# Performance work log

Measured on AMD Instinct MI355X. Metric: run time of the kernel, lower is better.

## Reference

```python
import jax, jax.numpy as jnp
import numpy as np

N_NODES = 100000
N_EDGES = 6400000
F_IN = 128
F_OUT = 16


def setup_inputs() -> dict:
    key = jax.random.key(0)
    k1, k2, k3 = jax.random.split(key, 3)
    x = jax.random.normal(k1, (N_NODES, F_IN), dtype=jnp.float32)
    edge_index = jax.random.randint(k2, (2, N_EDGES), 0, N_NODES, dtype=jnp.int64)
    W = jax.random.normal(k3, (F_IN, F_OUT), dtype=jnp.float32) / np.sqrt(F_IN)
    b = jnp.zeros((F_OUT,), dtype=jnp.float32)
    return {"x": x, "edge_index": edge_index, "W": W, "b": b}


def reference(x, edge_index, W, b):
    # GCNConv (PyG defaults: add self-loops, symmetric normalization) -> tanh -> mean pool
    N = x.shape[0]
    loops = jnp.arange(N, dtype=edge_index.dtype)
    row = jnp.concatenate([edge_index[0], loops])  # source nodes
    col = jnp.concatenate([edge_index[1], loops])  # target nodes
    # degree of target nodes (edge weight 1.0)
    deg = jax.ops.segment_sum(jnp.ones(row.shape[0], dtype=x.dtype), col, num_segments=N)
    dinv = jnp.where(deg > 0, jax.lax.rsqrt(deg), 0.0)
    norm = dinv[row] * dinv[col]  # [E+N]
    h = x @ W  # [N, F_OUT] transform first (cheaper than transforming messages)
    msgs = h[row] * norm[:, None]  # gather + scale
    out = jax.ops.segment_sum(msgs, col, num_segments=N) + b  # scatter-add
    h = jnp.tanh(out)
    # MeanAggregation over all nodes -> single graph embedding [1, F_OUT]
    return jnp.mean(h, axis=0, keepdims=True)
```

## Files before the change

kernel.cpp:

```cpp
#include <hip/hip_runtime.h>
#include <math.h>

#define N_NODES 100000
#define N_EDGES 6400000
#define F_IN 128
#define F_OUT 16
#define NB 391
#define NBLK 1600
#define EPB 4000
#define LOCW 392
#define KPB 4
#define ACCN (NB * 256 * F_OUT)
#define QSCALE 1024.0f
#define QINV   (1.0f / 1024.0f)
#define FIN_GRID 640

__global__ void __launch_bounds__(256) count_kernel(const int* __restrict__ col,
                                                    int* __restrict__ loc,
                                                    int* __restrict__ deg) {
    __shared__ int hist[NB];
    const int t = threadIdx.x, k = blockIdx.x;
    const int z0 = k * 63;
    for (int j = t; j < 63; j += 256)
        if (z0 + j < N_NODES) deg[z0 + j] = 0;
    for (int i = t; i < NB; i += 256) hist[i] = 0;
    __syncthreads();
    const int e0 = k * EPB;
    for (int i = t; i < EPB; i += 256) atomicAdd(&hist[col[e0 + i] >> 8], 1);
    __syncthreads();
    for (int b = t; b < NB; b += 256) loc[k * LOCW + b] = hist[b];
}

__global__ void __launch_bounds__(256) desta_kernel(const int* __restrict__ loc,
        int* __restrict__ destT, int* __restrict__ total) {
    __shared__ int tsum[256];
    const int t = threadIdx.x, b = blockIdx.x;
    int v[7]; int s = 0;
    #pragma unroll
    for (int j = 0; j < 7; j++) {
        int k = t * 7 + j;
        v[j] = (k < NBLK) ? loc[k * LOCW + b] : 0;
        s += v[j];
    }
    tsum[t] = s;
    __syncthreads();
    for (int off = 1; off < 256; off <<= 1) {
        int a = (t >= off) ? tsum[t - off] : 0;
        __syncthreads();
        tsum[t] += a;
        __syncthreads();
    }
    int run = tsum[t] - s;
    #pragma unroll
    for (int j = 0; j < 7; j++) {
        int k = t * 7 + j;
        if (k < NBLK) destT[(size_t)b * NBLK + k] = run;
        run += v[j];
    }
    if (t == 255) total[b] = tsum[255];
}

__global__ void destb_kernel(const int* __restrict__ total, int* __restrict__ boffs) {
    __shared__ int lds[512];
    const int t = threadIdx.x;
    int v = (t < NB) ? total[t] : 0;
    lds[t] = v; __syncthreads();
    for (int off = 1; off < 512; off <<= 1) {
        int a = (t >= off) ? lds[t - off] : 0; __syncthreads();
        lds[t] += a; __syncthreads();
    }
    if (t < NB) boffs[t] = lds[t] - v;
    if (t == NB) boffs[NB] = N_EDGES;
}

__global__ void __launch_bounds__(256) place_kernel(const int* __restrict__ row,
        const int* __restrict__ col, const int* __restrict__ destT,
        const int* __restrict__ boffs, unsigned int* __restrict__ packed) {
    __shared__ int hist[NB];
    __shared__ int scanb[512];
    __shared__ int base[NB];
    __shared__ int gadj[NB];
    __shared__ unsigned int tile[EPB];
    __shared__ unsigned short tileb[EPB];
    const int t = threadIdx.x, k = blockIdx.x;
    const int e0 = k * EPB;
    int myc[16], myr[16];
    #pragma unroll
    for (int j = 0; j < 16; j++) {
        int idx = t + j * 256;
        if (idx < EPB) { myc[j] = col[e0 + idx]; myr[j] = row[e0 + idx]; }
        else { myc[j] = -1; myr[j] = 0; }
    }
    for (int i = t; i < NB; i += 256) hist[i] = 0;
    __syncthreads();
    #pragma unroll
    for (int j = 0; j < 16; j++)
        if (myc[j] >= 0) atomicAdd(&hist[myc[j] >> 8], 1);
    __syncthreads();
    scanb[t] = (t < NB) ? hist[t] : 0;
    scanb[t + 256] = (t + 256 < NB) ? hist[t + 256] : 0;
    __syncthreads();
    for (int off = 1; off < 512; off <<= 1) {
        int a  = (t >= off) ? scanb[t - off] : 0;
        int a2 = scanb[t + 256 - off];
        __syncthreads();
        scanb[t] += a; scanb[t + 256] += a2;
        __syncthreads();
    }
    if (t < NB) base[t] = scanb[t] - hist[t];
    if (t + 256 < NB) base[t + 256] = scanb[t + 256] - hist[t + 256];
    __syncthreads();
    for (int bb = t; bb < NB; bb += 256) {
        gadj[bb] = boffs[bb] + destT[(size_t)bb * NBLK + k] - base[bb];
        hist[bb] = 0;
    }
    __syncthreads();
    #pragma unroll
    for (int j = 0; j < 16; j++) {
        if (myc[j] >= 0) {
            int bb = myc[j] >> 8;
            int pos = base[bb] + atomicAdd(&hist[bb], 1);
            tile[pos] = ((unsigned)myr[j] << 8) | (unsigned)(myc[j] & 255);
            tileb[pos] = (unsigned short)bb;
        }
    }
    __syncthreads();
    for (int i = t; i < EPB; i += 256)
        packed[gadj[tileb[i]] + i] = tile[i];
}

__global__ void __launch_bounds__(256) deg_kernel(const unsigned int* __restrict__ packed,
        const int* __restrict__ boffs, int* __restrict__ deg) {
    __shared__ int dh[256];
    const int t = threadIdx.x;
    dh[t] = 0;
    __syncthreads();
    const int b = blockIdx.x, part = blockIdx.y;
    const int s = boffs[b], e = boffs[b + 1];
    const int chunk = (e - s + 3) >> 2;
    const int cs = s + part * chunk;
    const int ce = min(cs + chunk, e);
    for (int i = cs + t; i < ce; i += 256)
        atomicAdd(&dh[packed[i] & 255u], 1);
    __syncthreads();
    const int node = (b << 8) + t;
    if (node < N_NODES && dh[t]) atomicAdd(&deg[node], dh[t]);
}

__global__ void __launch_bounds__(256) gemm_kernel(const float* __restrict__ x,
        const float* __restrict__ W, const int* __restrict__ deg,
        short* __restrict__ gq) {
    __shared__ float Ws[F_IN * F_OUT];
    __shared__ float xs[16 * 132];
    const int tid = threadIdx.x;
    const int n0 = blockIdx.x * 16;
    const float4* W4 = (const float4*)W;
    for (int i = tid; i < 512; i += 256) ((float4*)Ws)[i] = W4[i];
    const float4* x4 = (const float4*)(x + (size_t)n0 * F_IN);
    for (int i = tid; i < 512; i += 256) {
        int n = i >> 5, j = i & 31;
        *(float4*)(xs + n * 132 + j * 4) = x4[i];
    }
    __syncthreads();
    const int node = tid >> 4, f = tid & 15;
    const float* xr = &xs[node * 132];
    float acc = 0.f;
    #pragma unroll 8
    for (int k = 0; k < F_IN; k++) acc += xr[k] * Ws[k * 16 + f];
    const float dinvn = rsqrtf((float)deg[n0 + node] + 1.0f);
    float v = acc * dinvn * QSCALE;
    v = fminf(fmaxf(v, -32000.f), 32000.f);
    gq[n0 * 16 + tid] = (short)__float2int_rn(v);
}

__global__ void __launch_bounds__(256) scatter_kernel(
        const unsigned int* __restrict__ packed, const int* __restrict__ boffs,
        const short* __restrict__ gq, int* __restrict__ accp) {
    __shared__ int sacc[256 * F_OUT];
    const int t = threadIdx.x;
    for (int i = t; i < 256 * F_OUT; i += 256) sacc[i] = 0;
    __syncthreads();
    const int b = blockIdx.x, part = blockIdx.y;
    const int s = boffs[b], e = boffs[b + 1];
    const int chunk = (e - s + KPB - 1) / KPB;
    const int cs = s + part * chunk;
    const int ce = min(cs + chunk, e);
    const int f = t & 15, eg = t >> 4;
    int i = cs + eg;
    for (; i + 48 < ce; i += 64) {
        unsigned p0 = packed[i];
        unsigned p1 = packed[i + 16];
        unsigned p2 = packed[i + 32];
        unsigned p3 = packed[i + 48];
        int v0 = gq[(p0 >> 8) * 16 + f];
        int v1 = gq[(p1 >> 8) * 16 + f];
        int v2 = gq[(p2 >> 8) * 16 + f];
        int v3 = gq[(p3 >> 8) * 16 + f];
        atomicAdd(&sacc[((p0 & 255u) << 4) + f], v0);
        atomicAdd(&sacc[((p1 & 255u) << 4) + f], v1);
        atomicAdd(&sacc[((p2 & 255u) << 4) + f], v2);
        atomicAdd(&sacc[((p3 & 255u) << 4) + f], v3);
    }
    for (; i < ce; i += 16) {
        unsigned p0 = packed[i];
        atomicAdd(&sacc[((p0 & 255u) << 4) + f], (int)gq[(p0 >> 8) * 16 + f]);
    }
    __syncthreads();
    const int nbase = b << 8;
    int* dst = accp + (size_t)part * ACCN + ((size_t)nbase << 4);
    for (int j = t; j < 256 * F_OUT; j += 256)
        if (nbase + (j >> 4) < N_NODES) dst[j] = sacc[j];
}

__global__ void __launch_bounds__(256) finalize_kernel(const int* __restrict__ accp,
        const short* __restrict__ gq, const int* __restrict__ deg,
        const float* __restrict__ b, double* __restrict__ dsum,
        int* __restrict__ done, float* __restrict__ out) {
    __shared__ float s[4][16];
    __shared__ int lastflag;
    const int tid = threadIdx.x;
    const int f = tid & 15;
    const float bf = b[f];
    float local = 0.f;
    for (int i = blockIdx.x * blockDim.x + tid; i < N_NODES * F_OUT;
         i += gridDim.x * blockDim.x) {
        const int n = i >> 4;
        int ai = accp[i] + accp[ACCN + i] + accp[2 * ACCN + i] + accp[3 * ACCN + i]
               + (int)gq[i];
        float dinvn = rsqrtf((float)deg[n] + 1.0f);
        local += tanhf(dinvn * ((float)ai * QINV) + bf);
    }
    local += __shfl_down(local, 32);
    local += __shfl_down(local, 16);
    const int lane = tid & 63, wave = tid >> 6;
    if (lane < 16) s[wave][lane] = local;
    __syncthreads();
    if (tid < 16) {
        float v = s[0][tid] + s[1][tid] + s[2][tid] + s[3][tid];
        atomicAdd(&dsum[tid], (double)v);
    }
    if (tid == 0) {
        __threadfence();
        lastflag = (atomicAdd(done, 1) == (int)gridDim.x - 1);
    }
    __syncthreads();
    if (lastflag && tid < 16) {
        double v = atomicAdd(&dsum[tid], 0.0);
        out[tid] = (float)(v * (1.0 / (double)N_NODES));
    }
}

extern "C" void kernel_launch(void* const* d_in, const int* in_sizes, int n_in,
                              void* d_out, int out_size, void* d_ws, size_t ws_size,
                              hipStream_t stream) {
    const float* x  = (const float*)d_in[0];
    const int*   ei = (const int*)d_in[1];
    const float* W  = (const float*)d_in[2];
    const float* b  = (const float*)d_in[3];
    float* out = (float*)d_out;

    const int* row = ei;
    const int* col = ei + N_EDGES;

    char* p = (char*)d_ws;
    double*       dsum   = (double*)p;        p += 16 * 8;
    int*          done   = (int*)p;           p += 16;
    int*          total  = (int*)p;           p += 1568;
    int*          boffs  = (int*)p;           p += (NB + 1) * 4;
    int*          deg    = (int*)p;           p += (size_t)N_NODES * 4;
    short*        gq     = (short*)p;         p += (size_t)N_NODES * F_OUT * 2;
    unsigned int* packed = (unsigned int*)p;  p += (size_t)N_EDGES * 4;
    char*         shared = p;
    int*          loc    = (int*)shared;
    int*          destT  = (int*)(shared + (size_t)NBLK * LOCW * 4);
    int*          accp   = (int*)shared;

    hipMemsetAsync(dsum, 0, 16 * 8 + 16, stream);

    count_kernel   <<<NBLK, 256, 0, stream>>>(col, loc, deg);
    desta_kernel   <<<NB, 256, 0, stream>>>(loc, destT, total);
    destb_kernel   <<<1, 512, 0, stream>>>(total, boffs);
    place_kernel   <<<NBLK, 256, 0, stream>>>(row, col, destT, boffs, packed);
    deg_kernel     <<<dim3(NB, 4), 256, 0, stream>>>(packed, boffs, deg);
    gemm_kernel    <<<N_NODES / 16, 256, 0, stream>>>(x, W, deg, gq);
    scatter_kernel <<<dim3(NB, KPB), 256, 0, stream>>>(packed, boffs, gq, accp);
    finalize_kernel<<<FIN_GRID, 256, 0, stream>>>(accp, gq, deg, b, dsum, done, out);
}
```

Before: 264.9 us.

## Fold bucket offset scan into desta, vectorize gemm and scatter loads

The separate single-block destb scan is merged into desta_kernel with a last-block-done counter, which removes one kernel launch. The gemm kernel transposes W in shared memory so the dot product can use float4 reads of both x and W. The scatter kernel reads packed edges as uint4 and pads the shared accumulator rows to 17 words to reduce bank conflicts. The done counter (done+1) depends on the initial memset covering it, and the fused path adds a threadfence plus atomic reads.

Result: slower. 278.3 us (+5.0%).

```diff
diff --git a/kernel.cpp b/kernel.cpp
--- a/kernel.cpp
+++ b/kernel.cpp
@@ -14,6 +14,7 @@
 #define QSCALE 1024.0f
 #define QINV   (1.0f / 1024.0f)
 #define FIN_GRID 640
+#define SACCW 17
 
 __global__ void __launch_bounds__(256) count_kernel(const int* __restrict__ col,
                                                     int* __restrict__ loc,
@@ -32,8 +33,10 @@
 }
 
 __global__ void __launch_bounds__(256) desta_kernel(const int* __restrict__ loc,
-        int* __restrict__ destT, int* __restrict__ total) {
+        int* __restrict__ destT, int* __restrict__ total, int* __restrict__ boffs,
+        int* __restrict__ done2) {
     __shared__ int tsum[256];
+    __shared__ int lastflag;
     const int t = threadIdx.x, b = blockIdx.x;
     int v[7]; int s = 0;
     #pragma unroll
@@ -57,20 +60,28 @@
         if (k < NBLK) destT[(size_t)b * NBLK + k] = run;
         run += v[j];
     }
-    if (t == 255) total[b] = tsum[255];
-}
-
-__global__ void destb_kernel(const int* __restrict__ total, int* __restrict__ boffs) {
-    __shared__ int lds[512];
-    const int t = threadIdx.x;
-    int v = (t < NB) ? total[t] : 0;
-    lds[t] = v; __syncthreads();
+    if (t == 255) atomicExch(&total[b], tsum[255]);
+    if (t == 0) {
+        __threadfence();
+        lastflag = (atomicAdd(done2, 1) == (int)gridDim.x - 1);
+    }
+    __syncthreads();
+    if (!lastflag) return;
+    __shared__ int scanb[512];
+    int v0 = (t < NB) ? atomicAdd(&total[t], 0) : 0;
+    int v1 = (t + 256 < NB) ? atomicAdd(&total[t + 256], 0) : 0;
+    scanb[t] = v0; scanb[t + 256] = v1;
+    __syncthreads();
     for (int off = 1; off < 512; off <<= 1) {
-        int a = (t >= off) ? lds[t - off] : 0; __syncthreads();
-        lds[t] += a; __syncthreads();
-    }
-    if (t < NB) boffs[t] = lds[t] - v;
-    if (t == NB) boffs[NB] = N_EDGES;
+        int a  = (t >= off) ? scanb[t - off] : 0;
+        int a2 = scanb[t + 256 - off];
+        __syncthreads();
+        scanb[t] += a; scanb[t + 256] += a2;
+        __syncthreads();
+    }
+    if (t < NB) boffs[t] = scanb[t] - v0;
+    if (t + 256 < NB) boffs[t + 256] = scanb[t + 256] - v1;
+    if (t == 0) boffs[NB] = N_EDGES;
 }
 
 __global__ void __launch_bounds__(256) place_kernel(const int* __restrict__ row,
@@ -150,12 +161,14 @@
 __global__ void __launch_bounds__(256) gemm_kernel(const float* __restrict__ x,
         const float* __restrict__ W, const int* __restrict__ deg,
         short* __restrict__ gq) {
-    __shared__ float Ws[F_IN * F_OUT];
+    __shared__ float Wt[16 * 132];
     __shared__ float xs[16 * 132];
     const int tid = threadIdx.x;
     const int n0 = blockIdx.x * 16;
-    const float4* W4 = (const float4*)W;
-    for (int i = tid; i < 512; i += 256) ((float4*)Ws)[i] = W4[i];
+    for (int i = tid; i < 2048; i += 256) {
+        int k = i >> 4, f2 = i & 15;
+        Wt[f2 * 132 + k] = W[i];
+    }
     const float4* x4 = (const float4*)(x + (size_t)n0 * F_IN);
     for (int i = tid; i < 512; i += 256) {
         int n = i >> 5, j = i & 31;
@@ -163,10 +176,14 @@
     }
     __syncthreads();
     const int node = tid >> 4, f = tid & 15;
-    const float* xr = &xs[node * 132];
+    const float4* xr4 = (const float4*)(xs + node * 132);
+    const float4* wr4 = (const float4*)(Wt + f * 132);
     float acc = 0.f;
     #pragma unroll 8
-    for (int k = 0; k < F_IN; k++) acc += xr[k] * Ws[k * 16 + f];
+    for (int k = 0; k < 32; k++) {
+        float4 a = xr4[k], w = wr4[k];
+        acc += a.x * w.x + a.y * w.y + a.z * w.z + a.w * w.w;
+    }
     const float dinvn = rsqrtf((float)deg[n0 + node] + 1.0f);
     float v = acc * dinvn * QSCALE;
     v = fminf(fmaxf(v, -32000.f), 32000.f);
@@ -176,9 +193,9 @@
 __global__ void __launch_bounds__(256) scatter_kernel(
         const unsigned int* __restrict__ packed, const int* __restrict__ boffs,
         const short* __restrict__ gq, int* __restrict__ accp) {
-    __shared__ int sacc[256 * F_OUT];
+    __shared__ int sacc[256 * SACCW];
     const int t = threadIdx.x;
-    for (int i = t; i < 256 * F_OUT; i += 256) sacc[i] = 0;
+    for (int i = t; i < 256 * SACCW; i += 256) sacc[i] = 0;
     __syncthreads();
     const int b = blockIdx.x, part = blockIdx.y;
     const int s = boffs[b], e = boffs[b + 1];
@@ -186,30 +203,36 @@
     const int cs = s + part * chunk;
     const int ce = min(cs + chunk, e);
     const int f = t & 15, eg = t >> 4;
-    int i = cs + eg;
-    for (; i + 48 < ce; i += 64) {
-        unsigned p0 = packed[i];
-        unsigned p1 = packed[i + 16];
-        unsigned p2 = packed[i + 32];
-        unsigned p3 = packed[i + 48];
-        int v0 = gq[(p0 >> 8) * 16 + f];
-        int v1 = gq[(p1 >> 8) * 16 + f];
-        int v2 = gq[(p2 >> 8) * 16 + f];
-        int v3 = gq[(p3 >> 8) * 16 + f];
-        atomicAdd(&sacc[((p0 & 255u) << 4) + f], v0);
-        atomicAdd(&sacc[((p1 & 255u) << 4) + f], v1);
-        atomicAdd(&sacc[((p2 & 255u) << 4) + f], v2);
-        atomicAdd(&sacc[((p3 & 255u) << 4) + f], v3);
-    }
-    for (; i < ce; i += 16) {
-        unsigned p0 = packed[i];
-        atomicAdd(&sacc[((p0 & 255u) << 4) + f], (int)gq[(p0 >> 8) * 16 + f]);
+    const int cs_al = (cs + 3) & ~3;
+    if (eg == 0) {
+        int pe = min(cs_al, ce);
+        for (int j = cs; j < pe; j++) {
+            unsigned p0 = packed[j];
+            atomicAdd(&sacc[(p0 & 255u) * SACCW + f], (int)gq[(p0 >> 8) * 16 + f]);
+        }
+    }
+    int i = cs_al + eg * 4;
+    for (; i + 3 < ce; i += 64) {
+        uint4 pk = *(const uint4*)(packed + i);
+        int v0 = gq[(pk.x >> 8) * 16 + f];
+        int v1 = gq[(pk.y >> 8) * 16 + f];
+        int v2 = gq[(pk.z >> 8) * 16 + f];
+        int v3 = gq[(pk.w >> 8) * 16 + f];
+        atomicAdd(&sacc[(pk.x & 255u) * SACCW + f], v0);
+        atomicAdd(&sacc[(pk.y & 255u) * SACCW + f], v1);
+        atomicAdd(&sacc[(pk.z & 255u) * SACCW + f], v2);
+        atomicAdd(&sacc[(pk.w & 255u) * SACCW + f], v3);
+    }
+    const int jend = min(ce, i + 4);
+    for (int j = i; j < jend; j++) {
+        unsigned p0 = packed[j];
+        atomicAdd(&sacc[(p0 & 255u) * SACCW + f], (int)gq[(p0 >> 8) * 16 + f]);
     }
     __syncthreads();
     const int nbase = b << 8;
     int* dst = accp + (size_t)part * ACCN + ((size_t)nbase << 4);
     for (int j = t; j < 256 * F_OUT; j += 256)
-        if (nbase + (j >> 4) < N_NODES) dst[j] = sacc[j];
+        if (nbase + (j >> 4) < N_NODES) dst[j] = sacc[(j >> 4) * SACCW + (j & 15)];
 }
 
 __global__ void __launch_bounds__(256) finalize_kernel(const int* __restrict__ accp,
@@ -278,8 +301,7 @@
     hipMemsetAsync(dsum, 0, 16 * 8 + 16, stream);
 
     count_kernel   <<<NBLK, 256, 0, stream>>>(col, loc, deg);
-    desta_kernel   <<<NB, 256, 0, stream>>>(loc, destT, total);
-    destb_kernel   <<<1, 512, 0, stream>>>(total, boffs);
+    desta_kernel   <<<NB, 256, 0, stream>>>(loc, destT, total, boffs, done + 1);
     place_kernel   <<<NBLK, 256, 0, stream>>>(row, col, destT, boffs, packed);
     deg_kernel     <<<dim3(NB, 4), 256, 0, stream>>>(packed, boffs, deg);
     gemm_kernel    <<<N_NODES / 16, 256, 0, stream>>>(x, W, deg, gq);
```
